# Performance work log

Measured on AMD Instinct MI355X. Metric: run time of the kernel, lower is better.

Reference implementation:

```python
import jax, jax.numpy as jnp
import numpy as np
from functools import reduce

N = 20          # total qubits
N_SQC = 4       # shadow-circuit qubits
REPEAT = 2      # BasicEntangleLayer repeat
CDTYPE = jnp.complex64

_I2 = jnp.eye(2, dtype=CDTYPE)
_X  = jnp.array([[0, 1], [1, 0]], dtype=CDTYPE)   # PauliX
_P0 = jnp.array([[1, 0], [0, 0]], dtype=CDTYPE)
_P1 = jnp.array([[0, 0], [0, 1]], dtype=CDTYPE)


def multi_kron(mats):
    return reduce(jnp.kron, mats)


def _ry(t):
    c = jnp.cos(t * 0.5).astype(CDTYPE)
    s = jnp.sin(t * 0.5).astype(CDTYPE)
    return jnp.stack([jnp.stack([c, -s]), jnp.stack([s, c])])


def _rz(t):
    e = jnp.exp(-0.5j * t.astype(CDTYPE))
    z = jnp.zeros((), CDTYPE)
    return jnp.stack([jnp.stack([e, z]), jnp.stack([z, jnp.conj(e)])])


def _yzy_layer(p, n):
    # per qubit i: Ry(p[3i]) then Rz(p[3i+1]) then Ry(p[3i+2])
    mats = [_ry(p[3 * i + 2]) @ _rz(p[3 * i + 1]) @ _ry(p[3 * i]) for i in range(n)]
    return multi_kron(mats)


def _cnot(c, t, n):
    a = [_I2] * n; a[c] = _P0
    b = [_I2] * n; b[c] = _P1; b[t] = _X
    return multi_kron(a) + multi_kron(b)


def _ring_of_cnot(n):
    U = jnp.eye(2 ** n, dtype=CDTYPE)
    for i in range(n):
        U = _cnot(i, (i + 1) % n, n) @ U
    return U


def build_circuit(weight):
    """BasicEntangleLayer (YZY rotations + ring of CNOTs, repeated) + final YZYLayer."""
    n = N_SQC
    ring = _ring_of_cnot(n)
    U = jnp.eye(2 ** n, dtype=CDTYPE)
    for r in range(REPEAT):
        p = weight[3 * n * r:3 * n * (r + 1)]
        U = ring @ (_yzy_layer(p, n) @ U)
    U = _yzy_layer(weight[3 * n * REPEAT:3 * n * (REPEAT + 1)], n) @ U
    return U


def setup_inputs() -> dict:
    key = jax.random.key(0)
    k1, k2 = jax.random.split(key)
    vector_batch = jax.random.normal(k1, (32, 2 ** N), dtype=jnp.float32)
    weight = jax.random.uniform(k2, (9 * N_SQC,), dtype=jnp.float32,
                                minval=0.0, maxval=2.0 * np.pi)
    return {"vector_batch": vector_batch, "weight": weight}


def reference(vector_batch, weight):
    B = vector_batch.shape[0]
    # row-wise L2 normalization, then amplitude encoding into 2^N complex state
    norm = jnp.linalg.norm(vector_batch, axis=1, keepdims=True)
    state = (vector_batch / jnp.maximum(norm, 1e-12)).astype(CDTYPE)  # (B, 2^N)

    U = build_circuit(weight)                        # (16, 16)
    M = multi_kron([_X] * N_SQC)                     # X^{\otimes n_sqc}
    temp = U.conj().T @ M @ U                        # (16, 16) Hermitian

    d = 2 ** N_SQC
    outs = []
    for q in range(N - N_SQC + 1):
        # apply temp locally on qubits [q, q+n_sqc): identical math to
        # <state| I^{\otimes q} (x) temp (x) I^{\otimes rest} |state>
        s = state.reshape(B, 2 ** q, d, -1)          # (B, left, 16, right)
        ts = jnp.einsum('ij,bajc->baic', temp, s)
        outs.append(jnp.einsum('bajc,bajc->b', s.conj(), ts).real)
    return jnp.stack(outs, axis=1).astype(jnp.float32)  # (B, N-n_sqc+1)
```

## Files before the change

### kernel.cpp

```cpp
#include <hip/hip_runtime.h>
#include <math.h>

#define WS_TU    0
#define WS_S     256
#define WS_N     800
#define WS_PART  1024
#define WS_NPART 35840
#define WS_NEED_BYTES ((WS_NPART + 2048) * 4)

typedef _Float16 half8 __attribute__((ext_vector_type(8)));
typedef float f32x4 __attribute__((ext_vector_type(4)));

__device__ inline float2 cmul2(float2 a, float2 b) {
  return make_float2(a.x * b.x - a.y * b.y, a.x * b.y + a.y * b.x);
}

__device__ inline int ringperm(int x) {
  if ((x >> 3) & 1) x ^= 4;
  if ((x >> 2) & 1) x ^= 2;
  if ((x >> 1) & 1) x ^= 1;
  if (x & 1)        x ^= 8;
  return x;
}

__device__ inline float2 yzy_elem(const float* wgt, int layer, int r, int c) {
  float2 prod = make_float2(1.f, 0.f);
#pragma unroll
  for (int k = 0; k < 4; k++) {
    float t0 = wgt[layer * 12 + 3 * k + 0];
    float t1 = wgt[layer * 12 + 3 * k + 1];
    float t2 = wgt[layer * 12 + 3 * k + 2];
    float s0, c0, s1, c1, s2, c2;
    sincosf(0.5f * t0, &s0, &c0);
    sincosf(0.5f * t1, &s1, &c1);
    sincosf(0.5f * t2, &s2, &c2);
    float A = c2 * c0, B = s2 * s0, C = c2 * s0, D = s2 * c0;
    float2 m00 = make_float2( c1 * (A - B), -s1 * (A + B));
    float2 m01 = make_float2(-c1 * (C + D),  s1 * (C - D));
    float2 m10 = make_float2( c1 * (C + D),  s1 * (C - D));
    float2 m11 = make_float2( c1 * (A - B),  s1 * (A + B));
    int rb = (r >> (3 - k)) & 1, cb = (c >> (3 - k)) & 1;
    float2 mm = rb ? (cb ? m11 : m10) : (cb ? m01 : m00);
    prod = cmul2(prod, mm);
  }
  return prod;
}

__global__ void build_T_kernel(const float* __restrict__ wgt, float* __restrict__ ws) {
  __shared__ float2 U[256], Y[256], W[256];
  const int t = threadIdx.x;
  const int r = t >> 4, c = t & 15;

  for (int k = t; k < 576; k += 256) ws[WS_S + k] = 0.f;

  U[t] = yzy_elem(wgt, 0, r, c);
  __syncthreads();
  W[ringperm(r) * 16 + c] = U[t];
  __syncthreads(); U[t] = W[t]; __syncthreads();
  Y[t] = yzy_elem(wgt, 1, r, c);
  __syncthreads();
  {
    float2 s = make_float2(0.f, 0.f);
#pragma unroll
    for (int k = 0; k < 16; k++) {
      float2 pr = cmul2(Y[r * 16 + k], U[k * 16 + c]);
      s.x += pr.x; s.y += pr.y;
    }
    W[t] = s;
  }
  __syncthreads(); U[t] = W[t]; __syncthreads();
  W[ringperm(r) * 16 + c] = U[t];
  __syncthreads(); U[t] = W[t]; __syncthreads();
  Y[t] = yzy_elem(wgt, 2, r, c);
  __syncthreads();
  {
    float2 s = make_float2(0.f, 0.f);
#pragma unroll
    for (int k = 0; k < 16; k++) {
      float2 pr = cmul2(Y[r * 16 + k], U[k * 16 + c]);
      s.x += pr.x; s.y += pr.y;
    }
    W[t] = s;
  }
  __syncthreads(); U[t] = W[t]; __syncthreads();
  Y[t] = U[(r ^ 15) * 16 + c];
  __syncthreads();
  float s_re = 0.f;
#pragma unroll
  for (int k = 0; k < 16; k++) {
    float2 u = U[k * 16 + r], m = Y[k * 16 + c];
    s_re += u.x * m.x + u.y * m.y;
  }
  ws[WS_TU + t] = s_re;
}

__device__ inline int swzB(int B) {
  int h = B >> 3;
  int f = (h ^ (h >> 3) ^ (h >> 6)) & 7;
  return B ^ f;
}

template <int P>
__device__ inline float windowM(const half8* __restrict__ HB, const float* __restrict__ Tr) {
  const int t = threadIdx.x;
  const int w = t >> 6, l = t & 63, g = l >> 4, i = l & 15;
  f32x4 hh[4] = {{0.f, 0.f, 0.f, 0.f}, {0.f, 0.f, 0.f, 0.f},
                 {0.f, 0.f, 0.f, 0.f}, {0.f, 0.f, 0.f, 0.f}};
#pragma unroll
  for (int s = 0; s < 2; s++) {
#pragma unroll
    for (int c = 0; c < 4; c++) {
      int rest = (w << 5) | ((s * 4 + c) << 2) | g;
      int rl = rest & ((1 << (P - 3)) - 1), rh = rest >> (P - 3);
      int pos = (rl << 3) | (i << P) | (rh << (P + 4));
      half8 fr = HB[swzB(pos >> 3)];
      hh[c] = __builtin_amdgcn_mfma_f32_16x16x32_f16(fr, fr, hh[c], 0, 0, 0);
    }
  }
  float part = 0.f;
#pragma unroll
  for (int reg = 0; reg < 4; reg++)
    part = fmaf(Tr[reg], (hh[0][reg] + hh[1][reg]) + (hh[2][reg] + hh[3][reg]), part);
  return part;
}

__global__ __launch_bounds__(256, 4) void passAll_kernel(const float* __restrict__ vb,
                                                         float* ws, int use_part) {
  __shared__ half8 HB[2048];
  const int t = threadIdx.x;
  const int bid = blockIdx.x;

  const int mode = (bid & 1) ? 2 : 0;
  const int idx = bid >> 1;
  const int b = idx >> 6, chunk = idx & 63;
  const int l = t & 63, g = (l >> 4) & 3, i = l & 15;

  float Treg[4];
#pragma unroll
  for (int reg = 0; reg < 4; reg++) Treg[reg] = ws[WS_TU + ((g * 4 + reg) << 4) + i];

  float part[11];
#pragma unroll
  for (int k = 0; k < 11; k++) part[k] = 0.f;

  float nsum = 0.f;
  if (mode == 0) {
    const float4* src4 = ((const float4*)vb) + ((size_t)b << 18) + ((size_t)chunk << 12);
    half8 h[8];
#pragma unroll
    for (int j = 0; j < 8; j++) {
      int B = j * 256 + t;
      float4 aa = src4[2 * B], cc = src4[2 * B + 1];
      nsum = fmaf(aa.x, aa.x, nsum); nsum = fmaf(aa.y, aa.y, nsum);
      nsum = fmaf(aa.z, aa.z, nsum); nsum = fmaf(aa.w, aa.w, nsum);
      nsum = fmaf(cc.x, cc.x, nsum); nsum = fmaf(cc.y, cc.y, nsum);
      nsum = fmaf(cc.z, cc.z, nsum); nsum = fmaf(cc.w, cc.w, nsum);
      half8 hh;
      hh[0] = (_Float16)aa.x; hh[1] = (_Float16)aa.y; hh[2] = (_Float16)aa.z; hh[3] = (_Float16)aa.w;
      hh[4] = (_Float16)cc.x; hh[5] = (_Float16)cc.y; hh[6] = (_Float16)cc.z; hh[7] = (_Float16)cc.w;
      h[j] = hh;
      HB[swzB(B)] = hh;
    }
    {
      f32x4 hh[4] = {{0.f, 0.f, 0.f, 0.f}, {0.f, 0.f, 0.f, 0.f},
                     {0.f, 0.f, 0.f, 0.f}, {0.f, 0.f, 0.f, 0.f}};
#pragma unroll
      for (int j = 0; j < 8; j++)
        hh[j & 3] = __builtin_amdgcn_mfma_f32_16x16x32_f16(h[j], h[j], hh[j & 3], 0, 0, 0);
      float p0 = 0.f;
#pragma unroll
      for (int reg = 0; reg < 4; reg++)
        p0 = fmaf(Treg[reg], (hh[0][reg] + hh[1][reg]) + (hh[2][reg] + hh[3][reg]), p0);
      part[0] = p0;
    }
  } else {
    const float4* src4 = ((const float4*)vb) + ((size_t)b << 18) + chunk * 8;
#pragma unroll
    for (int j = 0; j < 8; j++) {
      int B = j * 256 + t;
      int row = B >> 2;
      int c4 = (B & 3) * 2;
      float4 aa = src4[row * 512 + c4], cc = src4[row * 512 + c4 + 1];
      half8 hh;
      hh[0] = (_Float16)aa.x; hh[1] = (_Float16)aa.y; hh[2] = (_Float16)aa.z; hh[3] = (_Float16)aa.w;
      hh[4] = (_Float16)cc.x; hh[5] = (_Float16)cc.y; hh[6] = (_Float16)cc.z; hh[7] = (_Float16)cc.w;
      HB[swzB(B)] = hh;
    }
  }
  __syncthreads();

  if (mode == 0) {
    part[1] += windowM<4>(HB, Treg);
    part[2] += windowM<5>(HB, Treg);
    part[3] += windowM<6>(HB, Treg);
    part[4] += windowM<7>(HB, Treg);
    part[5] += windowM<8>(HB, Treg);
    part[6] += windowM<9>(HB, Treg);
    part[7] += windowM<10>(HB, Treg);
    half8 h2[8];
#pragma unroll
    for (int j = 0; j < 8; j++) h2[j] = HB[swzB(j * 256 + t)];
    __syncthreads();
#pragma unroll
    for (int e = 0; e < 8; e++) {
      half8 v;
#pragma unroll
      for (int j = 0; j < 8; j++) v[j] = h2[j][e];
      HB[swzB(8 * t + e)] = v;
    }
    __syncthreads();
    part[8]  += windowM<3>(HB, Treg);
    part[9]  += windowM<4>(HB, Treg);
    part[10] += windowM<5>(HB, Treg);
  } else {
    part[0] += windowM<5>(HB, Treg);
    part[1] += windowM<6>(HB, Treg);
    part[2] += windowM<7>(HB, Treg);
    part[3] += windowM<8>(HB, Treg);
    part[4] += windowM<9>(HB, Treg);
    part[5] += windowM<10>(HB, Treg);
  }
  __syncthreads();

  float* red2 = (float*)HB;
#pragma unroll
  for (int k = 0; k < 11; k++) red2[k * 256 + t] = part[k];
  red2[11 * 256 + t] = nsum;
  __syncthreads();

  const int win = t >> 4, idx16 = t & 15;
  const float4* r4 = (const float4*)red2;
  float4 q0 = r4[win * 64 + idx16],      q1 = r4[win * 64 + 16 + idx16];
  float4 q2 = r4[win * 64 + 32 + idx16], q3 = r4[win * 64 + 48 + idx16];
  float s1 = ((q0.x + q0.y) + (q0.z + q0.w)) + ((q1.x + q1.y) + (q1.z + q1.w)) +
             ((q2.x + q2.y) + (q2.z + q2.w)) + ((q3.x + q3.y) + (q3.z + q3.w));
#pragma unroll
  for (int off = 8; off; off >>= 1) s1 += __shfl_down(s1, off, 16);

  if (idx16 == 0) {
    if (mode == 0) {
      if (win < 11) {
        int q = (win < 8) ? (13 - win) : (24 - win);
        if (use_part) ws[WS_PART + (b * 17 + q) * 64 + chunk] = s1;
        else          atomicAdd(ws + WS_S + b * 17 + q, s1);
      } else if (win == 11) {
        if (use_part) ws[WS_NPART + b * 64 + chunk] = s1;
        else          atomicAdd(ws + WS_N + b, s1);
      }
    } else {
      if (win < 6) {
        int q = 5 - win;
        if (use_part) ws[WS_PART + (b * 17 + q) * 64 + chunk] = s1;
        else          atomicAdd(ws + WS_S + b * 17 + q, s1);
      }
    }
  }
}

__global__ void finalize_kernel(const float* __restrict__ ws, float* __restrict__ out,
                                int use_part) {
  int i = blockIdx.x * 256 + threadIdx.x;
  if (i < 544) {
    int b = i / 17;
    float s, n;
    if (use_part) {
      const float* sp = ws + WS_PART + i * 64;
      s = 0.f;
#pragma unroll 8
      for (int c = 0; c < 64; c++) s += sp[c];
      const float* np = ws + WS_NPART + b * 64;
      n = 0.f;
#pragma unroll 8
      for (int c = 0; c < 64; c++) n += np[c];
    } else {
      s = ws[WS_S + i];
      n = ws[WS_N + b];
    }
    out[i] = s / fmaxf(n, 1e-24f);
  }
}

extern "C" void kernel_launch(void* const* d_in, const int* in_sizes, int n_in,
                              void* d_out, int out_size, void* d_ws, size_t ws_size,
                              hipStream_t stream) {
  const float* vb  = (const float*)d_in[0];
  const float* wgt = (const float*)d_in[1];
  float* out = (float*)d_out;
  float* ws  = (float*)d_ws;
  int use_part = (ws_size >= (size_t)WS_NEED_BYTES) ? 1 : 0;

  build_T_kernel<<<1, 256, 0, stream>>>(wgt, ws);
  passAll_kernel<<<4096, 256, 0, stream>>>(vb, ws, use_part);
  finalize_kernel<<<3, 256, 0, stream>>>(ws, out, use_part);
}
```

Measured before the change: 59.93 us.

## Fuse circuit-matrix construction into main pass kernel and drop separate build launch

Removes the single-block build_T kernel and instead has every block of the main pass recompute the 16x16 observable matrix in shared memory, with the sincos values computed once per block into a table. This cuts a serialized tiny kernel launch and its global round-trip from the critical path. The zeroing of accumulators is now launched only when the partial-sum path is unused. In exchange, each of the 4096 blocks performs redundant small matrix products and many extra barriers before its main work.

```diff
diff --git a/kernel.cpp b/kernel.cpp
--- a/kernel.cpp
+++ b/kernel.cpp
@@ -1,7 +1,6 @@
 #include <hip/hip_runtime.h>
 #include <math.h>
 
-#define WS_TU    0
 #define WS_S     256
 #define WS_N     800
 #define WS_PART  1024
@@ -23,17 +22,15 @@
   return x;
 }
 
-__device__ inline float2 yzy_elem(const float* wgt, int layer, int r, int c) {
+__device__ inline float2 yzy_elem_tab(const float* scs, const float* ccs,
+                                      int layer, int r, int c) {
   float2 prod = make_float2(1.f, 0.f);
 #pragma unroll
   for (int k = 0; k < 4; k++) {
-    float t0 = wgt[layer * 12 + 3 * k + 0];
-    float t1 = wgt[layer * 12 + 3 * k + 1];
-    float t2 = wgt[layer * 12 + 3 * k + 2];
-    float s0, c0, s1, c1, s2, c2;
-    sincosf(0.5f * t0, &s0, &c0);
-    sincosf(0.5f * t1, &s1, &c1);
-    sincosf(0.5f * t2, &s2, &c2);
+    int base = layer * 12 + 3 * k;
+    float s0 = scs[base + 0], c0 = ccs[base + 0];
+    float s1 = scs[base + 1], c1 = ccs[base + 1];
+    float s2 = scs[base + 2], c2 = ccs[base + 2];
     float A = c2 * c0, B = s2 * s0, C = c2 * s0, D = s2 * c0;
     float2 m00 = make_float2( c1 * (A - B), -s1 * (A + B));
     float2 m01 = make_float2(-c1 * (C + D),  s1 * (C - D));
@@ -46,54 +43,6 @@
   return prod;
 }
 
-__global__ void build_T_kernel(const float* __restrict__ wgt, float* __restrict__ ws) {
-  __shared__ float2 U[256], Y[256], W[256];
-  const int t = threadIdx.x;
-  const int r = t >> 4, c = t & 15;
-
-  for (int k = t; k < 576; k += 256) ws[WS_S + k] = 0.f;
-
-  U[t] = yzy_elem(wgt, 0, r, c);
-  __syncthreads();
-  W[ringperm(r) * 16 + c] = U[t];
-  __syncthreads(); U[t] = W[t]; __syncthreads();
-  Y[t] = yzy_elem(wgt, 1, r, c);
-  __syncthreads();
-  {
-    float2 s = make_float2(0.f, 0.f);
-#pragma unroll
-    for (int k = 0; k < 16; k++) {
-      float2 pr = cmul2(Y[r * 16 + k], U[k * 16 + c]);
-      s.x += pr.x; s.y += pr.y;
-    }
-    W[t] = s;
-  }
-  __syncthreads(); U[t] = W[t]; __syncthreads();
-  W[ringperm(r) * 16 + c] = U[t];
-  __syncthreads(); U[t] = W[t]; __syncthreads();
-  Y[t] = yzy_elem(wgt, 2, r, c);
-  __syncthreads();
-  {
-    float2 s = make_float2(0.f, 0.f);
-#pragma unroll
-    for (int k = 0; k < 16; k++) {
-      float2 pr = cmul2(Y[r * 16 + k], U[k * 16 + c]);
-      s.x += pr.x; s.y += pr.y;
-    }
-    W[t] = s;
-  }
-  __syncthreads(); U[t] = W[t]; __syncthreads();
-  Y[t] = U[(r ^ 15) * 16 + c];
-  __syncthreads();
-  float s_re = 0.f;
-#pragma unroll
-  for (int k = 0; k < 16; k++) {
-    float2 u = U[k * 16 + r], m = Y[k * 16 + c];
-    s_re += u.x * m.x + u.y * m.y;
-  }
-  ws[WS_TU + t] = s_re;
-}
-
 __device__ inline int swzB(int B) {
   int h = B >> 3;
   int f = (h ^ (h >> 3) ^ (h >> 6)) & 7;
@@ -103,7 +52,7 @@
 template <int P>
 __device__ inline float windowM(const half8* __restrict__ HB, const float* __restrict__ Tr) {
   const int t = threadIdx.x;
-  const int w = t >> 6, l = t & 63, g = l >> 4, i = l & 15;
+  const int w = t >> 6, l = t & 63, g = (l >> 4) & 3, i = l & 15;
   f32x4 hh[4] = {{0.f, 0.f, 0.f, 0.f}, {0.f, 0.f, 0.f, 0.f},
                  {0.f, 0.f, 0.f, 0.f}, {0.f, 0.f, 0.f, 0.f}};
 #pragma unroll
@@ -124,7 +73,13 @@
   return part;
 }
 
+__global__ void init_zero_kernel(float* __restrict__ ws) {
+  int t = threadIdx.x;
+  for (int k = t; k < 576; k += 256) ws[WS_S + k] = 0.f;
+}
+
 __global__ __launch_bounds__(256, 4) void passAll_kernel(const float* __restrict__ vb,
+                                                         const float* __restrict__ wgt,
                                                          float* ws, int use_part) {
   __shared__ half8 HB[2048];
   const int t = threadIdx.x;
@@ -135,9 +90,68 @@
   const int b = idx >> 6, chunk = idx & 63;
   const int l = t & 63, g = (l >> 4) & 3, i = l & 15;
 
+  float* base = (float*)HB;
+  float2* Ub = (float2*)base;
+  float2* Yb = (float2*)(base + 512);
+  float2* Wb = (float2*)(base + 1024);
+  float* scs = base + 1536;
+  float* ccs = base + 1572;
+  float* Tsh = base + 1792;
+
+  if (t < 36) {
+    float s, c;
+    sincosf(0.5f * wgt[t], &s, &c);
+    scs[t] = s; ccs[t] = c;
+  }
+  __syncthreads();
+  {
+    const int r = t >> 4, c = t & 15;
+    Ub[t] = yzy_elem_tab(scs, ccs, 0, r, c);
+    __syncthreads();
+    Wb[ringperm(r) * 16 + c] = Ub[t];
+    __syncthreads(); Ub[t] = Wb[t]; __syncthreads();
+    Yb[t] = yzy_elem_tab(scs, ccs, 1, r, c);
+    __syncthreads();
+    {
+      float2 s = make_float2(0.f, 0.f);
+#pragma unroll
+      for (int k = 0; k < 16; k++) {
+        float2 pr = cmul2(Yb[r * 16 + k], Ub[k * 16 + c]);
+        s.x += pr.x; s.y += pr.y;
+      }
+      Wb[t] = s;
+    }
+    __syncthreads(); Ub[t] = Wb[t]; __syncthreads();
+    Wb[ringperm(r) * 16 + c] = Ub[t];
+    __syncthreads(); Ub[t] = Wb[t]; __syncthreads();
+    Yb[t] = yzy_elem_tab(scs, ccs, 2, r, c);
+    __syncthreads();
+    {
+      float2 s = make_float2(0.f, 0.f);
+#pragma unroll
+      for (int k = 0; k < 16; k++) {
+        float2 pr = cmul2(Yb[r * 16 + k], Ub[k * 16 + c]);
+        s.x += pr.x; s.y += pr.y;
+      }
+      Wb[t] = s;
+    }
+    __syncthreads(); Ub[t] = Wb[t]; __syncthreads();
+    Yb[t] = Ub[(r ^ 15) * 16 + c];
+    __syncthreads();
+    float s_re = 0.f;
+#pragma unroll
+    for (int k = 0; k < 16; k++) {
+      float2 u = Ub[k * 16 + r], m = Yb[k * 16 + c];
+      s_re += u.x * m.x + u.y * m.y;
+    }
+    Tsh[t] = s_re;
+  }
+  __syncthreads();
+
   float Treg[4];
 #pragma unroll
-  for (int reg = 0; reg < 4; reg++) Treg[reg] = ws[WS_TU + ((g * 4 + reg) << 4) + i];
+  for (int reg = 0; reg < 4; reg++) Treg[reg] = Tsh[((g * 4 + reg) << 4) + i];
+  __syncthreads();
 
   float part[11];
 #pragma unroll
@@ -289,7 +303,7 @@
   float* ws  = (float*)d_ws;
   int use_part = (ws_size >= (size_t)WS_NEED_BYTES) ? 1 : 0;
 
-  build_T_kernel<<<1, 256, 0, stream>>>(wgt, ws);
-  passAll_kernel<<<4096, 256, 0, stream>>>(vb, ws, use_part);
+  if (!use_part) init_zero_kernel<<<1, 256, 0, stream>>>(ws);
+  passAll_kernel<<<4096, 256, 0, stream>>>(vb, wgt, ws, use_part);
   finalize_kernel<<<3, 256, 0, stream>>>(ws, out, use_part);
 }
```

Measured after the change: 69.74 us. 16.4% more time.
